# Performance work log

Hardware: AMD Instinct MI355X
Metric: run time of the kernel (lower is better)

The kernel has to match this reference:

```python
import jax, jax.numpy as jnp
import numpy as np

HIDDEN = 2048
INTER = 768
N_EXPERTS = 16
TOP_K = 2
B, S = 4, 2048


def setup_inputs() -> dict:
    key = jax.random.key(0)
    ks = jax.random.split(key, 5)
    scale = 0.02
    return {
        "hidden_states": jax.random.normal(ks[0], (B, S, HIDDEN), dtype=jnp.float32),
        # nn.Linear weight layout: [out_features, in_features]
        "gate_w": jax.random.normal(ks[1], (N_EXPERTS, HIDDEN), dtype=jnp.float32) * scale,
        "w_gate": jax.random.normal(ks[2], (N_EXPERTS, INTER, HIDDEN), dtype=jnp.float32) * scale,
        "w_up": jax.random.normal(ks[3], (N_EXPERTS, INTER, HIDDEN), dtype=jnp.float32) * scale,
        "w_down": jax.random.normal(ks[4], (N_EXPERTS, HIDDEN, INTER), dtype=jnp.float32) * scale,
    }


def _moe_forward(hidden_states, gate_w, w_gate, w_up, w_down):
    b, s, h = hidden_states.shape
    x = hidden_states.reshape(-1, h)                      # [T, H]
    t = x.shape[0]
    logits = x @ gate_w.T                                 # [T, E]
    probs = jax.nn.softmax(logits, axis=-1)
    top_vals, top_idx = jax.lax.top_k(probs, TOP_K)       # [T, K]
    top_vals = top_vals / jnp.sum(top_vals, axis=-1, keepdims=True)
    # combine weights per token per expert (zero if not routed)
    comb = jnp.zeros((t, N_EXPERTS), dtype=x.dtype)
    comb = comb.at[jnp.arange(t)[:, None], top_idx].add(top_vals)  # [T, E]

    out = jnp.zeros_like(x)
    for e in range(N_EXPERTS):  # small fixed loop over experts
        g = x @ w_gate[e].T                               # [T, I]
        u = x @ w_up[e].T                                 # [T, I]
        y = (jax.nn.silu(g) * u) @ w_down[e].T            # [T, H]
        out = out + comb[:, e:e + 1] * y
    return out.reshape(b, s, h)


def reference(hidden_states, gate_w, w_gate, w_up, w_down):
    return _moe_forward(hidden_states, gate_w, w_gate, w_up, w_down)
```

## Files before the change

kernel.cpp:

```cpp
#include <hip/hip_runtime.h>
#include <hip/hip_bf16.h>

#define NTOK 8192
#define HID 2048
#define INTER 768
#define NEXP 16

typedef __bf16 bf16x8 __attribute__((ext_vector_type(8)));
typedef float f32x4 __attribute__((ext_vector_type(4)));

typedef const __attribute__((address_space(1))) void gvoid_t;
typedef __attribute__((address_space(3))) void lvoid_t;

static __device__ __forceinline__ void load_lds16(const void* g, void* l) {
  __builtin_amdgcn_global_load_lds((gvoid_t*)g, (lvoid_t*)l, 16, 0, 0);
}

static __device__ __forceinline__ unsigned short f2bf(float f) {
  unsigned int u = __float_as_uint(f);
  u += 0x7FFFu + ((u >> 16) & 1u);
  return (unsigned short)(u >> 16);
}

static __device__ __forceinline__ float bf2f(unsigned short b) {
  return __uint_as_float(((unsigned int)b) << 16);
}

__global__ __launch_bounds__(256) void cvt_kernel(const float* __restrict__ src,
                                                  unsigned short* __restrict__ dst, int n) {
  int i = (blockIdx.x * 256 + threadIdx.x) * 4;
  int stride = gridDim.x * 256 * 4;
  for (; i < n; i += stride) {
    float4 v = *reinterpret_cast<const float4*>(src + i);
    ushort4 o;
    o.x = f2bf(v.x); o.y = f2bf(v.y); o.z = f2bf(v.z); o.w = f2bf(v.w);
    *reinterpret_cast<ushort4*>(dst + i) = o;
  }
}

__global__ __launch_bounds__(256) void router_kernel(const float* __restrict__ x,
                                                     const float* __restrict__ gw,
                                                     int* __restrict__ te,
                                                     float* __restrict__ tw,
                                                     unsigned short* __restrict__ Xb) {
  const int lane = threadIdx.x & 63;
  const int wid = threadIdx.x >> 6;
  const int t0 = (blockIdx.x * 4 + wid) * 2;
  const float4* xa = reinterpret_cast<const float4*>(x + (size_t)t0 * HID);
  const float4* xb = xa + HID / 4;
  const float4* g4 = reinterpret_cast<const float4*>(gw);

  float4 va[8], vb[8];
#pragma unroll
  for (int j = 0; j < 8; ++j) {
    va[j] = xa[lane + 64 * j];
    vb[j] = xb[lane + 64 * j];
  }
  ushort4* oa = reinterpret_cast<ushort4*>(Xb + (size_t)t0 * HID);
  ushort4* ob = oa + HID / 4;
#pragma unroll
  for (int j = 0; j < 8; ++j) {
    ushort4 u;
    u.x = f2bf(va[j].x); u.y = f2bf(va[j].y); u.z = f2bf(va[j].z); u.w = f2bf(va[j].w);
    oa[lane + 64 * j] = u;
    u.x = f2bf(vb[j].x); u.y = f2bf(vb[j].y); u.z = f2bf(vb[j].z); u.w = f2bf(vb[j].w);
    ob[lane + 64 * j] = u;
  }

  float accA[NEXP], accB[NEXP];
#pragma unroll
  for (int e = 0; e < NEXP; ++e) { accA[e] = 0.f; accB[e] = 0.f; }
#pragma unroll
  for (int e = 0; e < NEXP; ++e) {
#pragma unroll
    for (int j = 0; j < 8; ++j) {
      float4 g = g4[e * (HID / 4) + lane + 64 * j];
      accA[e] += va[j].x * g.x + va[j].y * g.y + va[j].z * g.z + va[j].w * g.w;
      accB[e] += vb[j].x * g.x + vb[j].y * g.y + vb[j].z * g.z + vb[j].w * g.w;
    }
  }
#pragma unroll
  for (int e = 0; e < NEXP; ++e) {
#pragma unroll
    for (int m = 32; m >= 1; m >>= 1) {
      accA[e] += __shfl_xor(accA[e], m);
      accB[e] += __shfl_xor(accB[e], m);
    }
  }
  if (lane == 0) {
#pragma unroll
    for (int k = 0; k < 2; ++k) {
      const float* acc = k ? accB : accA;
      int t = t0 + k;
      float b0 = -1e30f; int i0 = 0;
#pragma unroll
      for (int e = 0; e < NEXP; ++e) { if (acc[e] > b0) { b0 = acc[e]; i0 = e; } }
      float b1 = -1e30f; int i1 = 0;
#pragma unroll
      for (int e = 0; e < NEXP; ++e) { if (e != i0 && acc[e] > b1) { b1 = acc[e]; i1 = e; } }
      float w0 = 1.f / (1.f + __expf(b1 - b0));
      te[2 * t] = i0; te[2 * t + 1] = i1;
      tw[2 * t] = w0; tw[2 * t + 1] = 1.f - w0;
    }
  }
}

__global__ __launch_bounds__(256) void build_kernel(
    const int* __restrict__ te, const float* __restrict__ tw,
    int* __restrict__ counts, int* __restrict__ offsets,
    int* __restrict__ tok_flat, float* __restrict__ w_flat,
    int* __restrict__ tok_slot,
    int* __restrict__ tile_map, int* __restrict__ n_tiles) {
  __shared__ int lds_cnt[NEXP][257];
  __shared__ int lds_off[NEXP];
  const int tid = threadIdx.x;
  const int lane = tid & 63;
  const int wv = tid >> 6;

  int cnt[NEXP];
#pragma unroll
  for (int ex = 0; ex < NEXP; ++ex) cnt[ex] = 0;
  for (int i = 0; i < 64; ++i) {
    int e = te[tid * 64 + i];
#pragma unroll
    for (int ex = 0; ex < NEXP; ++ex) cnt[ex] += (e == ex) ? 1 : 0;
  }
#pragma unroll
  for (int ex = 0; ex < NEXP; ++ex) lds_cnt[ex][tid] = cnt[ex];
  __syncthreads();

  for (int ex = wv * 4; ex < wv * 4 + 4; ++ex) {
    int carry = 0;
    for (int c = 0; c < 4; ++c) {
      int v = lds_cnt[ex][c * 64 + lane];
      int s = v;
#pragma unroll
      for (int d = 1; d < 64; d <<= 1) {
        int o = __shfl_up(s, d);
        if (lane >= d) s += o;
      }
      lds_cnt[ex][c * 64 + lane] = carry + s - v;
      carry += __shfl(s, 63);
    }
    if (lane == 0) lds_cnt[ex][256] = carry;
  }
  __syncthreads();

  if (tid == 0) {
    int run = 0, nt = 0;
    for (int e = 0; e < NEXP; ++e) {
      int tot = lds_cnt[e][256];
      counts[e] = tot;
      offsets[e] = run;
      lds_off[e] = run;
      for (int m0 = 0; m0 < tot; m0 += 128) tile_map[nt++] = (e << 16) | m0;
      run += tot;
    }
    *n_tiles = nt;
  }
  __syncthreads();

  int base[NEXP];
#pragma unroll
  for (int ex = 0; ex < NEXP; ++ex) base[ex] = lds_off[ex] + lds_cnt[ex][tid];
  for (int i = 0; i < 64; ++i) {
    int idx = tid * 64 + i;
    int e = te[idx];
    float w = tw[idx];
    int pos = 0;
#pragma unroll
    for (int ex = 0; ex < NEXP; ++ex) {
      if (e == ex) { pos = base[ex]; base[ex] = pos + 1; }
    }
    tok_flat[pos] = idx >> 1;
    w_flat[pos] = w;
    tok_slot[idx] = pos;
  }
}

#define EP_G 0
#define EP_U 1
#define EP_Y 2

template <int MODE, int NXB, int KD>
__global__ __launch_bounds__(256, 3) void gemm_kernel(
    const unsigned short* __restrict__ A,
    const unsigned short* __restrict__ Bw,
    const int* __restrict__ counts, const int* __restrict__ offsets,
    const int* __restrict__ tok_flat, const float* __restrict__ w_flat,
    const int* __restrict__ tile_map, const int* __restrict__ n_tiles,
    unsigned short* __restrict__ Hf, float* __restrict__ out) {
  const int bid = blockIdx.x;
  const int cpx = gridDim.x >> 3;
  const int wg = (bid & 7) * cpx + (bid >> 3);
  const int y = wg / NXB;
  if (y >= *n_tiles) return;
  const int xb = wg - y * NXB;
  const int tm = tile_map[y];
  const int e = tm >> 16, m0 = tm & 0xFFFF;
  const int cnt = counts[e];
  const int off = offsets[e];
  const int n0 = xb * 128;

  __shared__ __align__(16) unsigned short As0[128 * 32], As1[128 * 32];
  __shared__ __align__(16) unsigned short Bs0[128 * 32], Bs1[128 * 32];

  const int tid = threadIdx.x;
  const int lane = tid & 63;
  const int wid = tid >> 6;
  const int rl = tid >> 2;
  const int srcc = ((tid & 3) ^ ((tid >> 3) & 3)) * 8;
  const int d0 = tid * 8;
  const int d1 = d0 + 64 * 32;

  const int r0 = m0 + rl, r1 = r0 + 64;
  const int s0 = (r0 < cnt) ? off + r0 : off;
  const int s1 = (r1 < cnt) ? off + r1 : off;
  const unsigned short* aptr0;
  const unsigned short* aptr1;
  if (MODE == EP_Y) {
    aptr0 = A + (size_t)s0 * KD + srcc;
    aptr1 = A + (size_t)s1 * KD + srcc;
  } else {
    aptr0 = A + (size_t)tok_flat[s0] * KD + srcc;
    aptr1 = A + (size_t)tok_flat[s1] * KD + srcc;
  }
  const unsigned short* bptr0 = Bw + ((size_t)e * (NXB * 128) + n0 + rl) * KD + srcc;
  const unsigned short* bptr1 = bptr0 + (size_t)64 * KD;

  f32x4 zero = {0.f, 0.f, 0.f, 0.f};
  f32x4 acc[4][4];
#pragma unroll
  for (int i = 0; i < 4; ++i)
#pragma unroll
    for (int j = 0; j < 4; ++j) acc[i][j] = zero;

  const int wm = (wid >> 1) * 64;
  const int wn = (wid & 1) * 64;
  const int fr = lane & 15;
  const int cs = (((lane >> 4) ^ ((lane >> 1) & 3)) * 8);

#define STAGE(AS, BS, kt)                 \
  {                                       \
    load_lds16(aptr0 + (kt), (AS) + d0);  \
    load_lds16(aptr1 + (kt), (AS) + d1);  \
    load_lds16(bptr0 + (kt), (BS) + d0);  \
    load_lds16(bptr1 + (kt), (BS) + d1);  \
  }

#define COMPUTE(AS, BS)                                                                \
  {                                                                                    \
    bf16x8 af[4], bf_[4];                                                              \
    _Pragma("unroll") for (int i = 0; i < 4; ++i) {                                    \
      af[i] = *reinterpret_cast<const bf16x8*>((AS) + (wm + i * 16 + fr) * 32 + cs);   \
      bf_[i] = *reinterpret_cast<const bf16x8*>((BS) + (wn + i * 16 + fr) * 32 + cs);  \
    }                                                                                  \
    _Pragma("unroll") for (int i = 0; i < 4; ++i)                                      \
      _Pragma("unroll") for (int j = 0; j < 4; ++j)                                    \
        acc[i][j] = __builtin_amdgcn_mfma_f32_16x16x32_bf16(af[i], bf_[j], acc[i][j], 0, 0, 0); \
  }

#pragma unroll 1
  for (int kt = 0; kt < KD; kt += 64) {
    STAGE(As0, Bs0, kt);
    STAGE(As1, Bs1, kt + 32);
    __syncthreads();
    COMPUTE(As0, Bs0);
    COMPUTE(As1, Bs1);
    __syncthreads();
  }
#undef STAGE
#undef COMPUTE

  const int lr = (lane >> 4) * 4;
  const int lc = lane & 15;
#pragma unroll
  for (int i = 0; i < 4; ++i) {
#pragma unroll
    for (int r = 0; r < 4; ++r) {
      int m = wm + i * 16 + lr + r;
      if (m0 + m < cnt) {
        int slot = off + m0 + m;
        if (MODE == EP_G) {
          size_t base = (size_t)slot * INTER + (size_t)(n0 + wn + lc);
#pragma unroll
          for (int j = 0; j < 4; ++j) Hf[base + j * 16] = f2bf(acc[i][j][r]);
        } else if (MODE == EP_U) {
          size_t base = (size_t)slot * INTER + (size_t)(n0 + wn + lc);
#pragma unroll
          for (int j = 0; j < 4; ++j) {
            float g = bf2f(Hf[base + j * 16]);
            float u = acc[i][j][r];
            float h = g / (1.f + __expf(-g)) * u;
            Hf[base + j * 16] = f2bf(h);
          }
        } else {
          float w = w_flat[slot];
          size_t base = (size_t)slot * HID + (size_t)(n0 + wn + lc);
#pragma unroll
          for (int j = 0; j < 4; ++j) Hf[base + j * 16] = f2bf(w * acc[i][j][r]);
        }
      }
    }
  }
}

__global__ __launch_bounds__(256) void combine_kernel(const unsigned short* __restrict__ Yf,
                                                      const int* __restrict__ tok_slot,
                                                      float* __restrict__ out) {
  const int t = blockIdx.x;
  const int c = threadIdx.x * 8;
  const int s0 = tok_slot[2 * t];
  const int s1 = tok_slot[2 * t + 1];
  const ushort4* p0 = reinterpret_cast<const ushort4*>(Yf + (size_t)s0 * HID + c);
  const ushort4* p1 = reinterpret_cast<const ushort4*>(Yf + (size_t)s1 * HID + c);
  ushort4 a0 = p0[0], a1 = p0[1];
  ushort4 b0 = p1[0], b1 = p1[1];
  float4 o0, o1;
  o0.x = bf2f(a0.x) + bf2f(b0.x);
  o0.y = bf2f(a0.y) + bf2f(b0.y);
  o0.z = bf2f(a0.z) + bf2f(b0.z);
  o0.w = bf2f(a0.w) + bf2f(b0.w);
  o1.x = bf2f(a1.x) + bf2f(b1.x);
  o1.y = bf2f(a1.y) + bf2f(b1.y);
  o1.z = bf2f(a1.z) + bf2f(b1.z);
  o1.w = bf2f(a1.w) + bf2f(b1.w);
  float4* op = reinterpret_cast<float4*>(out + (size_t)t * HID + c);
  op[0] = o0;
  op[1] = o1;
}

extern "C" void kernel_launch(void* const* d_in, const int* in_sizes, int n_in,
                              void* d_out, int out_size, void* d_ws, size_t ws_size,
                              hipStream_t stream) {
  const float* x  = (const float*)d_in[0];
  const float* gw = (const float*)d_in[1];
  const float* wg = (const float*)d_in[2];
  const float* wu = (const float*)d_in[3];
  const float* wd = (const float*)d_in[4];
  float* out = (float*)d_out;
  char* ws = (char*)d_ws;

  int*   counts   = (int*)(ws + 0);
  int*   offsets  = (int*)(ws + 128);
  int*   n_tiles  = (int*)(ws + 192);
  int*   tile_map = (int*)(ws + 256);
  int*   te       = (int*)(ws + 1024);
  float* tw       = (float*)(ws + 66560);
  int*   tok_flat = (int*)(ws + 132096);
  float* w_flat   = (float*)(ws + 197632);
  unsigned short* Xb  = (unsigned short*)(ws + 263168);
  unsigned short* Wgb = (unsigned short*)(ws + 33817600);
  unsigned short* Wub = (unsigned short*)(ws + 84149248);
  unsigned short* Wdb = (unsigned short*)(ws + 134480896);
  unsigned short* Hf  = (unsigned short*)(ws + 184812544);
  int*   tok_slot = (int*)(ws + 209978368);
  unsigned short* Yf  = Wgb;

  cvt_kernel<<<2048, 256, 0, stream>>>(wg, Wgb, NEXP * INTER * HID);
  cvt_kernel<<<2048, 256, 0, stream>>>(wu, Wub, NEXP * INTER * HID);
  cvt_kernel<<<2048, 256, 0, stream>>>(wd, Wdb, NEXP * HID * INTER);

  router_kernel<<<NTOK / 8, 256, 0, stream>>>(x, gw, te, tw, Xb);
  build_kernel<<<1, 256, 0, stream>>>(te, tw, counts, offsets, tok_flat, w_flat,
                                      tok_slot, tile_map, n_tiles);

  gemm_kernel<EP_G, 6, HID><<<144 * 6, 256, 0, stream>>>(
      Xb, Wgb, counts, offsets, tok_flat, w_flat, tile_map, n_tiles, Hf, out);
  gemm_kernel<EP_U, 6, HID><<<144 * 6, 256, 0, stream>>>(
      Xb, Wub, counts, offsets, tok_flat, w_flat, tile_map, n_tiles, Hf, out);
  gemm_kernel<EP_Y, 16, INTER><<<144 * 16, 256, 0, stream>>>(
      Hf, Wdb, counts, offsets, tok_flat, w_flat, tile_map, n_tiles, Yf, out);
  combine_kernel<<<NTOK, 256, 0, stream>>>(Yf, tok_slot, out);
}
```

Measured before the change: 484.8 us.

## Fuse gate and up GEMMs into one kernel sharing the A tile

Merges the separate gate and up projection GEMMs into a single kernel. Each block loads the gathered token tile once and multiplies it against both weight tiles, keeping two accumulator sets, and applies SiLU*up in the epilogue. This removes one kernel launch, halves the activation gather traffic for these two GEMMs, and drops the bf16 round-trip of the gate result through Hf. In exchange it doubles accumulator registers and LDS per block, and occupancy is lowered to 2 blocks per CU.

```diff
diff --git a/kernel.cpp b/kernel.cpp
--- a/kernel.cpp
+++ b/kernel.cpp
@@ -178,24 +178,20 @@
   }
 }
 
-#define EP_G 0
-#define EP_U 1
-#define EP_Y 2
-
-template <int MODE, int NXB, int KD>
-__global__ __launch_bounds__(256, 3) void gemm_kernel(
-    const unsigned short* __restrict__ A,
-    const unsigned short* __restrict__ Bw,
+__global__ __launch_bounds__(256, 2) void gemm_gu_kernel(
+    const unsigned short* __restrict__ Xb,
+    const unsigned short* __restrict__ Wg,
+    const unsigned short* __restrict__ Wu,
     const int* __restrict__ counts, const int* __restrict__ offsets,
-    const int* __restrict__ tok_flat, const float* __restrict__ w_flat,
+    const int* __restrict__ tok_flat,
     const int* __restrict__ tile_map, const int* __restrict__ n_tiles,
-    unsigned short* __restrict__ Hf, float* __restrict__ out) {
+    unsigned short* __restrict__ Hf) {
   const int bid = blockIdx.x;
   const int cpx = gridDim.x >> 3;
   const int wg = (bid & 7) * cpx + (bid >> 3);
-  const int y = wg / NXB;
+  const int y = wg / 6;
   if (y >= *n_tiles) return;
-  const int xb = wg - y * NXB;
+  const int xb = wg - y * 6;
   const int tm = tile_map[y];
   const int e = tm >> 16, m0 = tm & 0xFFFF;
   const int cnt = counts[e];
@@ -203,7 +199,8 @@
   const int n0 = xb * 128;
 
   __shared__ __align__(16) unsigned short As0[128 * 32], As1[128 * 32];
-  __shared__ __align__(16) unsigned short Bs0[128 * 32], Bs1[128 * 32];
+  __shared__ __align__(16) unsigned short Bg0[128 * 32], Bg1[128 * 32];
+  __shared__ __align__(16) unsigned short Bu0[128 * 32], Bu1[128 * 32];
 
   const int tid = threadIdx.x;
   const int lane = tid & 63;
@@ -216,31 +213,134 @@
   const int r0 = m0 + rl, r1 = r0 + 64;
   const int s0 = (r0 < cnt) ? off + r0 : off;
   const int s1 = (r1 < cnt) ? off + r1 : off;
-  const unsigned short* aptr0;
-  const unsigned short* aptr1;
-  if (MODE == EP_Y) {
-    aptr0 = A + (size_t)s0 * KD + srcc;
-    aptr1 = A + (size_t)s1 * KD + srcc;
-  } else {
-    aptr0 = A + (size_t)tok_flat[s0] * KD + srcc;
-    aptr1 = A + (size_t)tok_flat[s1] * KD + srcc;
-  }
-  const unsigned short* bptr0 = Bw + ((size_t)e * (NXB * 128) + n0 + rl) * KD + srcc;
-  const unsigned short* bptr1 = bptr0 + (size_t)64 * KD;
+  const unsigned short* aptr0 = Xb + (size_t)tok_flat[s0] * HID + srcc;
+  const unsigned short* aptr1 = Xb + (size_t)tok_flat[s1] * HID + srcc;
+  const unsigned short* gptr0 = Wg + ((size_t)e * INTER + n0 + rl) * HID + srcc;
+  const unsigned short* gptr1 = gptr0 + (size_t)64 * HID;
+  const unsigned short* uptr0 = Wu + ((size_t)e * INTER + n0 + rl) * HID + srcc;
+  const unsigned short* uptr1 = uptr0 + (size_t)64 * HID;
 
   f32x4 zero = {0.f, 0.f, 0.f, 0.f};
-  f32x4 acc[4][4];
+  f32x4 accG[4][4], accU[4][4];
 #pragma unroll
   for (int i = 0; i < 4; ++i)
 #pragma unroll
-    for (int j = 0; j < 4; ++j) acc[i][j] = zero;
+    for (int j = 0; j < 4; ++j) { accG[i][j] = zero; accU[i][j] = zero; }
 
   const int wm = (wid >> 1) * 64;
   const int wn = (wid & 1) * 64;
   const int fr = lane & 15;
   const int cs = (((lane >> 4) ^ ((lane >> 1) & 3)) * 8);
 
-#define STAGE(AS, BS, kt)                 \
+#define STAGE_GU(AS, BGS, BUS, kt)           \
+  {                                          \
+    load_lds16(aptr0 + (kt), (AS) + d0);     \
+    load_lds16(aptr1 + (kt), (AS) + d1);     \
+    load_lds16(gptr0 + (kt), (BGS) + d0);    \
+    load_lds16(gptr1 + (kt), (BGS) + d1);    \
+    load_lds16(uptr0 + (kt), (BUS) + d0);    \
+    load_lds16(uptr1 + (kt), (BUS) + d1);    \
+  }
+
+#define COMPUTE_GU(AS, BGS, BUS)                                                       \
+  {                                                                                    \
+    bf16x8 af[4], bg[4], bu[4];                                                        \
+    _Pragma("unroll") for (int i = 0; i < 4; ++i) {                                    \
+      af[i] = *reinterpret_cast<const bf16x8*>((AS) + (wm + i * 16 + fr) * 32 + cs);   \
+      bg[i] = *reinterpret_cast<const bf16x8*>((BGS) + (wn + i * 16 + fr) * 32 + cs);  \
+      bu[i] = *reinterpret_cast<const bf16x8*>((BUS) + (wn + i * 16 + fr) * 32 + cs);  \
+    }                                                                                  \
+    _Pragma("unroll") for (int i = 0; i < 4; ++i)                                      \
+      _Pragma("unroll") for (int j = 0; j < 4; ++j) {                                  \
+        accG[i][j] = __builtin_amdgcn_mfma_f32_16x16x32_bf16(af[i], bg[j], accG[i][j], 0, 0, 0); \
+        accU[i][j] = __builtin_amdgcn_mfma_f32_16x16x32_bf16(af[i], bu[j], accU[i][j], 0, 0, 0); \
+      }                                                                                \
+  }
+
+#pragma unroll 1
+  for (int kt = 0; kt < HID; kt += 64) {
+    STAGE_GU(As0, Bg0, Bu0, kt);
+    STAGE_GU(As1, Bg1, Bu1, kt + 32);
+    __syncthreads();
+    COMPUTE_GU(As0, Bg0, Bu0);
+    COMPUTE_GU(As1, Bg1, Bu1);
+    __syncthreads();
+  }
+#undef STAGE_GU
+#undef COMPUTE_GU
+
+  const int lr = (lane >> 4) * 4;
+  const int lc = lane & 15;
+#pragma unroll
+  for (int i = 0; i < 4; ++i) {
+#pragma unroll
+    for (int r = 0; r < 4; ++r) {
+      int m = wm + i * 16 + lr + r;
+      if (m0 + m < cnt) {
+        size_t base = (size_t)(off + m0 + m) * INTER + (size_t)(n0 + wn + lc);
+#pragma unroll
+        for (int j = 0; j < 4; ++j) {
+          float g = accG[i][j][r];
+          float u = accU[i][j][r];
+          float h = g / (1.f + __expf(-g)) * u;
+          Hf[base + j * 16] = f2bf(h);
+        }
+      }
+    }
+  }
+}
+
+__global__ __launch_bounds__(256, 3) void gemm_y_kernel(
+    const unsigned short* __restrict__ Hf,
+    const unsigned short* __restrict__ Wd,
+    const int* __restrict__ counts, const int* __restrict__ offsets,
+    const float* __restrict__ w_flat,
+    const int* __restrict__ tile_map, const int* __restrict__ n_tiles,
+    unsigned short* __restrict__ Yf) {
+  const int bid = blockIdx.x;
+  const int cpx = gridDim.x >> 3;
+  const int wg = (bid & 7) * cpx + (bid >> 3);
+  const int y = wg / 16;
+  if (y >= *n_tiles) return;
+  const int xb = wg - y * 16;
+  const int tm = tile_map[y];
+  const int e = tm >> 16, m0 = tm & 0xFFFF;
+  const int cnt = counts[e];
+  const int off = offsets[e];
+  const int n0 = xb * 128;
+
+  __shared__ __align__(16) unsigned short As0[128 * 32], As1[128 * 32];
+  __shared__ __align__(16) unsigned short Bs0[128 * 32], Bs1[128 * 32];
+
+  const int tid = threadIdx.x;
+  const int lane = tid & 63;
+  const int wid = tid >> 6;
+  const int rl = tid >> 2;
+  const int srcc = ((tid & 3) ^ ((tid >> 3) & 3)) * 8;
+  const int d0 = tid * 8;
+  const int d1 = d0 + 64 * 32;
+
+  const int r0 = m0 + rl, r1 = r0 + 64;
+  const int s0 = (r0 < cnt) ? off + r0 : off;
+  const int s1 = (r1 < cnt) ? off + r1 : off;
+  const unsigned short* aptr0 = Hf + (size_t)s0 * INTER + srcc;
+  const unsigned short* aptr1 = Hf + (size_t)s1 * INTER + srcc;
+  const unsigned short* bptr0 = Wd + ((size_t)e * HID + n0 + rl) * INTER + srcc;
+  const unsigned short* bptr1 = bptr0 + (size_t)64 * INTER;
+
+  f32x4 zero = {0.f, 0.f, 0.f, 0.f};
+  f32x4 acc[4][4];
+#pragma unroll
+  for (int i = 0; i < 4; ++i)
+#pragma unroll
+    for (int j = 0; j < 4; ++j) acc[i][j] = zero;
+
+  const int wm = (wid >> 1) * 64;
+  const int wn = (wid & 1) * 64;
+  const int fr = lane & 15;
+  const int cs = (((lane >> 4) ^ ((lane >> 1) & 3)) * 8);
+
+#define STAGE_Y(AS, BS, kt)               \
   {                                       \
     load_lds16(aptr0 + (kt), (AS) + d0);  \
     load_lds16(aptr1 + (kt), (AS) + d1);  \
@@ -248,7 +348,7 @@
     load_lds16(bptr1 + (kt), (BS) + d1);  \
   }
 
-#define COMPUTE(AS, BS)                                                                \
+#define COMPUTE_Y(AS, BS)                                                              \
   {                                                                                    \
     bf16x8 af[4], bf_[4];                                                              \
     _Pragma("unroll") for (int i = 0; i < 4; ++i) {                                    \
@@ -261,16 +361,16 @@
   }
 
 #pragma unroll 1
-  for (int kt = 0; kt < KD; kt += 64) {
-    STAGE(As0, Bs0, kt);
-    STAGE(As1, Bs1, kt + 32);
+  for (int kt = 0; kt < INTER; kt += 64) {
+    STAGE_Y(As0, Bs0, kt);
+    STAGE_Y(As1, Bs1, kt + 32);
     __syncthreads();
-    COMPUTE(As0, Bs0);
-    COMPUTE(As1, Bs1);
+    COMPUTE_Y(As0, Bs0);
+    COMPUTE_Y(As1, Bs1);
     __syncthreads();
   }
-#undef STAGE
-#undef COMPUTE
+#undef STAGE_Y
+#undef COMPUTE_Y
 
   const int lr = (lane >> 4) * 4;
   const int lc = lane & 15;
@@ -281,25 +381,10 @@
       int m = wm + i * 16 + lr + r;
       if (m0 + m < cnt) {
         int slot = off + m0 + m;
-        if (MODE == EP_G) {
-          size_t base = (size_t)slot * INTER + (size_t)(n0 + wn + lc);
-#pragma unroll
-          for (int j = 0; j < 4; ++j) Hf[base + j * 16] = f2bf(acc[i][j][r]);
-        } else if (MODE == EP_U) {
-          size_t base = (size_t)slot * INTER + (size_t)(n0 + wn + lc);
-#pragma unroll
-          for (int j = 0; j < 4; ++j) {
-            float g = bf2f(Hf[base + j * 16]);
-            float u = acc[i][j][r];
-            float h = g / (1.f + __expf(-g)) * u;
-            Hf[base + j * 16] = f2bf(h);
-          }
-        } else {
-          float w = w_flat[slot];
-          size_t base = (size_t)slot * HID + (size_t)(n0 + wn + lc);
-#pragma unroll
-          for (int j = 0; j < 4; ++j) Hf[base + j * 16] = f2bf(w * acc[i][j][r]);
-        }
+        float w = w_flat[slot];
+        size_t base = (size_t)slot * HID + (size_t)(n0 + wn + lc);
+#pragma unroll
+        for (int j = 0; j < 4; ++j) Yf[base + j * 16] = f2bf(w * acc[i][j][r]);
       }
     }
   }
@@ -365,11 +450,9 @@
   build_kernel<<<1, 256, 0, stream>>>(te, tw, counts, offsets, tok_flat, w_flat,
                                       tok_slot, tile_map, n_tiles);
 
-  gemm_kernel<EP_G, 6, HID><<<144 * 6, 256, 0, stream>>>(
-      Xb, Wgb, counts, offsets, tok_flat, w_flat, tile_map, n_tiles, Hf, out);
-  gemm_kernel<EP_U, 6, HID><<<144 * 6, 256, 0, stream>>>(
-      Xb, Wub, counts, offsets, tok_flat, w_flat, tile_map, n_tiles, Hf, out);
-  gemm_kernel<EP_Y, 16, INTER><<<144 * 16, 256, 0, stream>>>(
-      Hf, Wdb, counts, offsets, tok_flat, w_flat, tile_map, n_tiles, Yf, out);
+  gemm_gu_kernel<<<144 * 6, 256, 0, stream>>>(
+      Xb, Wgb, Wub, counts, offsets, tok_flat, tile_map, n_tiles, Hf);
+  gemm_y_kernel<<<144 * 16, 256, 0, stream>>>(
+      Hf, Wdb, counts, offsets, w_flat, tile_map, n_tiles, Yf);
   combine_kernel<<<NTOK, 256, 0, stream>>>(Yf, tok_slot, out);
 }
```

New measurement: 449.8 us. 7.2% less time.
